# Kernel tuning notes

Hardware: AMD Instinct MI355X
Metric: run time of the kernel (lower is better)

The kernel has to match this reference:

```python
import jax, jax.numpy as jnp
import numpy as np
import math

SIZE = 64
NLAND = 8
N_ITER = 6


def setup_inputs() -> dict:
    key = jax.random.key(0)
    k1, k2, k3 = jax.random.split(key, 3)
    B, T, C = 4, 4096, 1024
    return {
        "q": jax.random.normal(k1, (B, T, C), dtype=jnp.float32),
        "k": jax.random.normal(k2, (B, T, C), dtype=jnp.float32),
        "v": jax.random.normal(k3, (B, T, C), dtype=jnp.float32),
    }


def _iterative_pinv(mat, n_iter=N_ITER):
    # Newton-Schulz iteration for pseudo-inverse of [..., m, m] kernel.
    m = mat.shape[-1]
    I = jnp.eye(m, dtype=mat.dtype)
    K = mat
    # NOTE: torch.max over the whole tensor (global scalar), faithful to source.
    V = (1.0 / jnp.max(jnp.sum(K, axis=-2))) * jnp.swapaxes(K, -1, -2)
    for _ in range(n_iter):
        KV = jnp.matmul(K, V)
        V = jnp.matmul(0.25 * V, 13.0 * I - jnp.matmul(KV, 15.0 * I - jnp.matmul(KV, 7.0 * I - KV)))
    return V


def reference(q, k, v):
    B, T, C = q.shape
    H = C // SIZE
    scale = 1.0 / math.sqrt(SIZE)
    # Faithful reshape (not transpose) as in the source module.
    qh = q.reshape(B, H, T, SIZE)
    kh = k.reshape(B, H, T, SIZE)
    vh = v.reshape(B, H, T, SIZE)
    # T % NLAND == 0 branch: landmark = segment mean over T//NLAND tokens.
    q_l = qh.reshape(B, H, NLAND, T // NLAND, SIZE).mean(axis=-2)  # [B,H,m,d]
    k_l = kh.reshape(B, H, NLAND, T // NLAND, SIZE).mean(axis=-2)
    kernel_1 = jax.nn.softmax(jnp.einsum('bhtd,bhmd->bhtm', qh, k_l) * scale, axis=-1)  # [B,H,T,m]
    kernel_2 = jax.nn.softmax(jnp.einsum('bhmd,bhnd->bhmn', q_l, k_l) * scale, axis=-1)  # [B,H,m,m]
    kernel_3 = jax.nn.softmax(jnp.einsum('bhmd,bhtd->bhmt', q_l, kh) * scale, axis=-1)  # [B,H,m,T]
    pinv = _iterative_pinv(kernel_2)  # [B,H,m,m]
    k3v = jnp.matmul(kernel_3, vh)    # [B,H,m,d]
    out = jnp.matmul(jnp.matmul(kernel_1, pinv), k3v)  # [B,H,T,d]
    return out.reshape(B, T, C)
```

## Files before the change

### kernel.cpp

```cpp
#include <hip/hip_runtime.h>
#include <math.h>

#define T_TOK 4096
#define DD 64
#define NHEADS 64
#define SEG 512
#define SCALE 0.125f

#define QL_OFF   0
#define KL_OFF   32768
#define K2_OFF   65536
#define CS_OFF   69632
#define KP_OFF   70144
#define PA_OFF   332288
#define PD_OFF   2429440
#define W2_OFF   2462208

#define WAVE_BAR() __builtin_amdgcn_wave_barrier()

__global__ __launch_bounds__(256) void qsum_kernel(
    const float* __restrict__ q, float* __restrict__ ws) {
  int tid = threadIdx.x;
  const float4* q4 = (const float4*)q + (size_t)blockIdx.x * 8192;
  float4 b[2][8];
#pragma unroll
  for (int i = 0; i < 8; ++i) b[0][i] = q4[i * 256 + tid];
  float4 a = make_float4(0.f, 0.f, 0.f, 0.f);
#pragma unroll
  for (int j = 0; j < 4; ++j) {
    if (j < 3) {
#pragma unroll
      for (int i = 0; i < 8; ++i)
        b[(j + 1) & 1][i] = q4[(j + 1) * 2048 + i * 256 + tid];
    }
#pragma unroll
    for (int i = 0; i < 8; ++i) {
      float4 x = b[j & 1][i];
      a.x += x.x; a.y += x.y; a.z += x.z; a.w += x.w;
    }
  }
  __shared__ float4 red[16][17];
  red[tid >> 4][tid & 15] = a;
  __syncthreads();
  if (tid < 16) {
    float4 s = make_float4(0.f, 0.f, 0.f, 0.f);
#pragma unroll
    for (int g = 0; g < 16; ++g) {
      float4 r = red[g][tid];
      s.x += r.x; s.y += r.y; s.z += r.z; s.w += r.w;
    }
    const float inv = 1.f / (float)SEG;
    s.x *= inv; s.y *= inv; s.z *= inv; s.w *= inv;
    ((float4*)(ws + QL_OFF))[blockIdx.x * 16 + tid] = s;
  }
}

__global__ __launch_bounds__(256) void kvpass_kernel(
    const float* __restrict__ k, const float* __restrict__ v,
    float* __restrict__ ws) {
  int tid = threadIdx.x;
  int w = tid >> 6, lane = tid & 63;
  int gw = blockIdx.x * 4 + w;
  int hb = gw >> 6;
  __shared__ float qls[8][68];
  __shared__ float kt_all[4][16][68];
  __shared__ float pl_all[4][16][9];
  float (*kt)[68] = kt_all[w];
  float (*pl)[9]  = pl_all[w];

  if (tid < 128) {
    float4 x = ((const float4*)(ws + QL_OFF))[hb * 128 + tid];
    *(float4*)&qls[tid >> 4][(tid & 15) * 4] = x;
  }
  __syncthreads();

  int m = lane & 7, g = lane >> 4;
  size_t tokbase = (size_t)gw * 64;
  const float4* k4 = (const float4*)k + tokbase * 16;
  const float4* v4 = (const float4*)v + tokbase * 16;
  float4 kb[2][4], vb[2][4];
#pragma unroll
  for (int i = 0; i < 4; ++i) { kb[0][i] = k4[i * 64 + lane]; vb[0][i] = v4[i * 64 + lane]; }

  float4 ks = make_float4(0.f, 0.f, 0.f, 0.f);
  float den = 0.f;
  float4 acc[8];
#pragma unroll
  for (int mm = 0; mm < 8; ++mm) acc[mm] = make_float4(0.f, 0.f, 0.f, 0.f);

#pragma unroll
  for (int tile = 0; tile < 4; ++tile) {
    int cur = tile & 1;
    if (tile < 3) {
#pragma unroll
      for (int i = 0; i < 4; ++i) {
        kb[cur ^ 1][i] = k4[(tile + 1) * 256 + i * 64 + lane];
        vb[cur ^ 1][i] = v4[(tile + 1) * 256 + i * 64 + lane];
      }
    }
#pragma unroll
    for (int i = 0; i < 4; ++i) {
      int f4 = i * 64 + lane;
      *(float4*)&kt[f4 >> 4][(f4 & 15) * 4] = kb[cur][i];
      ks.x += kb[cur][i].x; ks.y += kb[cur][i].y;
      ks.z += kb[cur][i].z; ks.w += kb[cur][i].w;
    }
    WAVE_BAR();
#pragma unroll
    for (int rep = 0; rep < 2; ++rep) {
      int t = rep * 8 + (lane >> 3);
      const float4* kr = (const float4*)&kt[t][0];
      const float4* qr = (const float4*)&qls[m][0];
      float dp = 0.f;
#pragma unroll
      for (int d4 = 0; d4 < 16; ++d4) {
        float4 kv = kr[d4], qv = qr[d4];
        dp += kv.x * qv.x + kv.y * qv.y + kv.z * qv.z + kv.w * qv.w;
      }
      float p = __expf(dp * SCALE);
      pl[t][m] = p;
      den += p;
    }
    WAVE_BAR();
#pragma unroll
    for (int i = 0; i < 4; ++i) {
      int t = i * 4 + g;
      float4 vv = vb[cur][i];
      float p0 = pl[t][0], p1 = pl[t][1], p2 = pl[t][2], p3 = pl[t][3];
      float p4 = pl[t][4], p5 = pl[t][5], p6 = pl[t][6], p7 = pl[t][7];
      acc[0].x += p0 * vv.x; acc[0].y += p0 * vv.y; acc[0].z += p0 * vv.z; acc[0].w += p0 * vv.w;
      acc[1].x += p1 * vv.x; acc[1].y += p1 * vv.y; acc[1].z += p1 * vv.z; acc[1].w += p1 * vv.w;
      acc[2].x += p2 * vv.x; acc[2].y += p2 * vv.y; acc[2].z += p2 * vv.z; acc[2].w += p2 * vv.w;
      acc[3].x += p3 * vv.x; acc[3].y += p3 * vv.y; acc[3].z += p3 * vv.z; acc[3].w += p3 * vv.w;
      acc[4].x += p4 * vv.x; acc[4].y += p4 * vv.y; acc[4].z += p4 * vv.z; acc[4].w += p4 * vv.w;
      acc[5].x += p5 * vv.x; acc[5].y += p5 * vv.y; acc[5].z += p5 * vv.z; acc[5].w += p5 * vv.w;
      acc[6].x += p6 * vv.x; acc[6].y += p6 * vv.y; acc[6].z += p6 * vv.z; acc[6].w += p6 * vv.w;
      acc[7].x += p7 * vv.x; acc[7].y += p7 * vv.y; acc[7].z += p7 * vv.z; acc[7].w += p7 * vv.w;
    }
    WAVE_BAR();
  }
  ks.x += __shfl_xor(ks.x, 16, 64); ks.y += __shfl_xor(ks.y, 16, 64);
  ks.z += __shfl_xor(ks.z, 16, 64); ks.w += __shfl_xor(ks.w, 16, 64);
  ks.x += __shfl_xor(ks.x, 32, 64); ks.y += __shfl_xor(ks.y, 32, 64);
  ks.z += __shfl_xor(ks.z, 32, 64); ks.w += __shfl_xor(ks.w, 32, 64);
  if (lane < 16)
    ((float4*)(ws + KP_OFF))[gw * 16 + lane] = ks;
  den += __shfl_xor(den, 8, 64);
  den += __shfl_xor(den, 16, 64);
  den += __shfl_xor(den, 32, 64);
  if (lane < 8)
    ws[PD_OFF + (size_t)gw * 8 + lane] = den;
#pragma unroll
  for (int mm = 0; mm < 8; ++mm) {
#pragma unroll
    for (int s = 16; s <= 32; s <<= 1) {
      acc[mm].x += __shfl_xor(acc[mm].x, s, 64);
      acc[mm].y += __shfl_xor(acc[mm].y, s, 64);
      acc[mm].z += __shfl_xor(acc[mm].z, s, 64);
      acc[mm].w += __shfl_xor(acc[mm].w, s, 64);
    }
  }
  if (lane < 16) {
#pragma unroll
    for (int mm = 0; mm < 8; ++mm)
      ((float4*)(ws + PA_OFF))[((size_t)gw * 8 + mm) * 16 + lane] = acc[mm];
  }
}

__global__ __launch_bounds__(512) void prepk_kernel(float* __restrict__ ws) {
  int hb = blockIdx.x, tid = threadIdx.x;
  __shared__ float qls[8][68];
  __shared__ float kls[8][68];
  __shared__ float ee[8][9];
  int m = tid >> 6, d = tid & 63;
  float s = 0.f;
#pragma unroll
  for (int j = 0; j < 8; ++j)
    s += ws[KP_OFF + (size_t)(hb * 64 + m * 8 + j) * 64 + d];
  s *= (1.f / (float)SEG);
  kls[m][d] = s;
  ws[KL_OFF + hb * 512 + tid] = s;
  qls[m][d] = ws[QL_OFF + hb * 512 + tid];
  __syncthreads();
  if (tid < 64) {
    int i = tid >> 3, j = tid & 7;
    float dot = 0.f;
#pragma unroll
    for (int dd = 0; dd < 64; ++dd) dot += qls[i][dd] * kls[j][dd];
    ee[i][j] = __expf(dot * SCALE);
  }
  __syncthreads();
  if (tid < 64) {
    int i = tid >> 3, j = tid & 7;
    float ssum = 0.f;
#pragma unroll
    for (int jj = 0; jj < 8; ++jj) ssum += ee[i][jj];
    ws[K2_OFF + hb * 64 + tid] = ee[i][j] / ssum;
  }
  if (tid < 8) {
    float cs = 0.f;
    for (int ii = 0; ii < 8; ++ii) {
      float ssum = 0.f;
#pragma unroll
      for (int jj = 0; jj < 8; ++jj) ssum += ee[ii][jj];
      cs += ee[ii][tid] / ssum;
    }
    ws[CS_OFF + hb * 8 + tid] = cs;
  }
}

__global__ __launch_bounds__(512) void pinvw2_kernel(float* __restrict__ ws) {
  int hb = blockIdx.x, tid = threadIdx.x;
  __shared__ float k3vs[8][68];
  __shared__ float K[8][9], V[8][9], X[8][9], Y[8][9];
  __shared__ float smax;
  int m = tid >> 6, d = tid & 63;
  float s = 0.f, den = 0.f;
  for (int c = 0; c < 64; ++c) {
    s += ws[PA_OFF + (((size_t)hb * 64 + c) * 8 + m) * 64 + d];
    den += ws[PD_OFF + ((size_t)hb * 64 + c) * 8 + m];
  }
  k3vs[m][d] = s / den;
  if (tid < 64) {
    float mx = 0.f;
    for (int t = 0; t < 8; ++t) mx = fmaxf(mx, ws[CS_OFF + t * 64 + tid]);
    for (int off = 32; off; off >>= 1) mx = fmaxf(mx, __shfl_xor(mx, off, 64));
    if (tid == 0) smax = mx;
  }
  int i = (tid >> 3) & 7, j = tid & 7;
  if (tid < 64) K[i][j] = ws[K2_OFF + hb * 64 + tid];
  __syncthreads();
  if (tid < 64) V[i][j] = K[j][i] * (1.f / smax);
  __syncthreads();
  for (int it = 0; it < 6; ++it) {
    float x = 0.f;
    if (tid < 64) {
      for (int kk = 0; kk < 8; ++kk) x += K[i][kk] * V[kk][j];
      X[i][j] = x;
    }
    __syncthreads();
    float bm = 0.f;
    if (tid < 64) {
      for (int kk = 0; kk < 8; ++kk) bm += X[i][kk] * X[kk][j];
      bm = 7.f * x - bm;
      Y[i][j] = bm;
    }
    __syncthreads();
    float dm = 0.f;
    if (tid < 64) {
      for (int kk = 0; kk < 8; ++kk) dm += X[i][kk] * Y[kk][j];
      dm = 15.f * x - dm;
    }
    __syncthreads();
    if (tid < 64) Y[i][j] = dm;
    __syncthreads();
    float vd = 0.f;
    if (tid < 64) {
      for (int kk = 0; kk < 8; ++kk) vd += V[i][kk] * Y[kk][j];
      vd = 0.25f * (13.f * V[i][j] - vd);
    }
    __syncthreads();
    if (tid < 64) V[i][j] = vd;
    __syncthreads();
  }
  float o = 0.f;
#pragma unroll
  for (int jj = 0; jj < 8; ++jj) o += V[m][jj] * k3vs[jj][d];
  ws[W2_OFF + hb * 512 + tid] = o;
}

__global__ __launch_bounds__(256) void out_kernel(
    const float* __restrict__ q, float* __restrict__ out,
    const float* __restrict__ ws) {
  int tid = threadIdx.x;
  int w = tid >> 6, lane = tid & 63;
  int gw = blockIdx.x * 4 + w;
  int hb = gw >> 6;
  __shared__ float qt_all[4][16][68];
  __shared__ float pl_all[4][16][9];
  __shared__ float w2_all[4][8][68];
  float (*qt)[68] = qt_all[w];
  float (*pl)[9]  = pl_all[w];
  float (*w2)[68] = w2_all[w];

  int m = lane & 7;
  float4 klrow[16];
#pragma unroll
  for (int d4 = 0; d4 < 16; ++d4)
    klrow[d4] = ((const float4*)(ws + KL_OFF))[hb * 128 + m * 16 + d4];
#pragma unroll
  for (int i = 0; i < 2; ++i) {
    int f4 = i * 64 + lane;
    float4 y = ((const float4*)(ws + W2_OFF))[hb * 128 + f4];
    *(float4*)&w2[f4 >> 4][(f4 & 15) * 4] = y;
  }

  size_t base4 = (size_t)gw * 1024;
  const float4* q4 = (const float4*)q + base4;
  float4* o4 = (float4*)out + base4;
  float4 buf[2][4];
#pragma unroll
  for (int i = 0; i < 4; ++i) buf[0][i] = q4[i * 64 + lane];

#pragma unroll
  for (int tile = 0; tile < 4; ++tile) {
    int cur = tile & 1;
    if (tile < 3) {
#pragma unroll
      for (int i = 0; i < 4; ++i)
        buf[cur ^ 1][i] = q4[(tile + 1) * 256 + i * 64 + lane];
    }
#pragma unroll
    for (int i = 0; i < 4; ++i) {
      int f4 = i * 64 + lane;
      *(float4*)&qt[f4 >> 4][(f4 & 15) * 4] = buf[cur][i];
    }
    WAVE_BAR();
#pragma unroll
    for (int rep = 0; rep < 2; ++rep) {
      int t = rep * 8 + (lane >> 3);
      const float4* qr = (const float4*)&qt[t][0];
      float dot = 0.f;
#pragma unroll
      for (int d4 = 0; d4 < 16; ++d4) {
        float4 a = qr[d4];
        dot += a.x * klrow[d4].x + a.y * klrow[d4].y +
               a.z * klrow[d4].z + a.w * klrow[d4].w;
      }
      pl[t][m] = __expf(dot * SCALE);
    }
    WAVE_BAR();
#pragma unroll
    for (int i = 0; i < 4; ++i) {
      int t = i * 4 + (lane >> 4);
      int qd = lane & 15;
      float p0 = pl[t][0], p1 = pl[t][1], p2 = pl[t][2], p3 = pl[t][3];
      float p4 = pl[t][4], p5 = pl[t][5], p6 = pl[t][6], p7 = pl[t][7];
      float inv = 1.f / (p0 + p1 + p2 + p3 + p4 + p5 + p6 + p7);
      float4 acc = make_float4(0.f, 0.f, 0.f, 0.f);
      float pm[8] = {p0, p1, p2, p3, p4, p5, p6, p7};
#pragma unroll
      for (int m2 = 0; m2 < 8; ++m2) {
        float wgt = pm[m2] * inv;
        float4 wv = *(const float4*)&w2[m2][qd * 4];
        acc.x += wgt * wv.x; acc.y += wgt * wv.y;
        acc.z += wgt * wv.z; acc.w += wgt * wv.w;
      }
      o4[tile * 256 + i * 64 + lane] = acc;
    }
    WAVE_BAR();
  }
}

extern "C" void kernel_launch(void* const* d_in, const int* in_sizes, int n_in,
                              void* d_out, int out_size, void* d_ws, size_t ws_size,
                              hipStream_t stream) {
  const float* q = (const float*)d_in[0];
  const float* k = (const float*)d_in[1];
  const float* v = (const float*)d_in[2];
  float* out = (float*)d_out;
  float* ws = (float*)d_ws;

  qsum_kernel<<<512, 256, 0, stream>>>(q, ws);
  kvpass_kernel<<<1024, 256, 0, stream>>>(k, v, ws);
  prepk_kernel<<<NHEADS, 512, 0, stream>>>(ws);
  pinvw2_kernel<<<NHEADS, 512, 0, stream>>>(ws);
  out_kernel<<<1024, 256, 0, stream>>>(q, out, ws);
}
```

Before: 99.14 us.

## Stage V through LDS and remap P·V accumulation to avoid cross-lane reductions

Result: slower. 116.6 us (+17.6%).

```diff
diff --git a/kernel.cpp b/kernel.cpp
--- a/kernel.cpp
+++ b/kernel.cpp
@@ -64,8 +64,10 @@
   int hb = gw >> 6;
   __shared__ float qls[8][68];
   __shared__ float kt_all[4][16][68];
+  __shared__ float vt_all[4][16][68];
   __shared__ float pl_all[4][16][9];
   float (*kt)[68] = kt_all[w];
+  float (*vt)[68] = vt_all[w];
   float (*pl)[9]  = pl_all[w];
 
   if (tid < 128) {
@@ -74,36 +76,35 @@
   }
   __syncthreads();
 
-  int m = lane & 7, g = lane >> 4;
+  int m = lane & 7, g = lane >> 4, d4i = lane & 15;
   size_t tokbase = (size_t)gw * 64;
   const float4* k4 = (const float4*)k + tokbase * 16;
   const float4* v4 = (const float4*)v + tokbase * 16;
-  float4 kb[2][4], vb[2][4];
-#pragma unroll
-  for (int i = 0; i < 4; ++i) { kb[0][i] = k4[i * 64 + lane]; vb[0][i] = v4[i * 64 + lane]; }
+
+  float4 kb[4], vb[4];
+#pragma unroll
+  for (int i = 0; i < 4; ++i) { kb[i] = k4[i * 64 + lane]; vb[i] = v4[i * 64 + lane]; }
 
   float4 ks = make_float4(0.f, 0.f, 0.f, 0.f);
   float den = 0.f;
-  float4 acc[8];
-#pragma unroll
-  for (int mm = 0; mm < 8; ++mm) acc[mm] = make_float4(0.f, 0.f, 0.f, 0.f);
+  float4 acc0 = make_float4(0.f, 0.f, 0.f, 0.f);
+  float4 acc1 = make_float4(0.f, 0.f, 0.f, 0.f);
 
 #pragma unroll
   for (int tile = 0; tile < 4; ++tile) {
-    int cur = tile & 1;
-    if (tile < 3) {
-#pragma unroll
-      for (int i = 0; i < 4; ++i) {
-        kb[cur ^ 1][i] = k4[(tile + 1) * 256 + i * 64 + lane];
-        vb[cur ^ 1][i] = v4[(tile + 1) * 256 + i * 64 + lane];
-      }
-    }
 #pragma unroll
     for (int i = 0; i < 4; ++i) {
       int f4 = i * 64 + lane;
-      *(float4*)&kt[f4 >> 4][(f4 & 15) * 4] = kb[cur][i];
-      ks.x += kb[cur][i].x; ks.y += kb[cur][i].y;
-      ks.z += kb[cur][i].z; ks.w += kb[cur][i].w;
+      *(float4*)&kt[f4 >> 4][(f4 & 15) * 4] = kb[i];
+      *(float4*)&vt[f4 >> 4][(f4 & 15) * 4] = vb[i];
+      ks.x += kb[i].x; ks.y += kb[i].y; ks.z += kb[i].z; ks.w += kb[i].w;
+    }
+    if (tile < 3) {
+#pragma unroll
+      for (int i = 0; i < 4; ++i) {
+        kb[i] = k4[(tile + 1) * 256 + i * 64 + lane];
+        vb[i] = v4[(tile + 1) * 256 + i * 64 + lane];
+      }
     }
     WAVE_BAR();
 #pragma unroll
@@ -123,19 +124,12 @@
     }
     WAVE_BAR();
 #pragma unroll
-    for (int i = 0; i < 4; ++i) {
-      int t = i * 4 + g;
-      float4 vv = vb[cur][i];
-      float p0 = pl[t][0], p1 = pl[t][1], p2 = pl[t][2], p3 = pl[t][3];
-      float p4 = pl[t][4], p5 = pl[t][5], p6 = pl[t][6], p7 = pl[t][7];
-      acc[0].x += p0 * vv.x; acc[0].y += p0 * vv.y; acc[0].z += p0 * vv.z; acc[0].w += p0 * vv.w;
-      acc[1].x += p1 * vv.x; acc[1].y += p1 * vv.y; acc[1].z += p1 * vv.z; acc[1].w += p1 * vv.w;
-      acc[2].x += p2 * vv.x; acc[2].y += p2 * vv.y; acc[2].z += p2 * vv.z; acc[2].w += p2 * vv.w;
-      acc[3].x += p3 * vv.x; acc[3].y += p3 * vv.y; acc[3].z += p3 * vv.z; acc[3].w += p3 * vv.w;
-      acc[4].x += p4 * vv.x; acc[4].y += p4 * vv.y; acc[4].z += p4 * vv.z; acc[4].w += p4 * vv.w;
-      acc[5].x += p5 * vv.x; acc[5].y += p5 * vv.y; acc[5].z += p5 * vv.z; acc[5].w += p5 * vv.w;
-      acc[6].x += p6 * vv.x; acc[6].y += p6 * vv.y; acc[6].z += p6 * vv.z; acc[6].w += p6 * vv.w;
-      acc[7].x += p7 * vv.x; acc[7].y += p7 * vv.y; acc[7].z += p7 * vv.z; acc[7].w += p7 * vv.w;
+    for (int t = 0; t < 16; ++t) {
+      float4 vv = *(const float4*)&vt[t][d4i * 4];
+      float pa = pl[t][g];
+      float pb = pl[t][g + 4];
+      acc0.x += pa * vv.x; acc0.y += pa * vv.y; acc0.z += pa * vv.z; acc0.w += pa * vv.w;
+      acc1.x += pb * vv.x; acc1.y += pb * vv.y; acc1.z += pb * vv.z; acc1.w += pb * vv.w;
     }
     WAVE_BAR();
   }
@@ -150,21 +144,8 @@
   den += __shfl_xor(den, 32, 64);
   if (lane < 8)
     ws[PD_OFF + (size_t)gw * 8 + lane] = den;
-#pragma unroll
-  for (int mm = 0; mm < 8; ++mm) {
-#pragma unroll
-    for (int s = 16; s <= 32; s <<= 1) {
-      acc[mm].x += __shfl_xor(acc[mm].x, s, 64);
-      acc[mm].y += __shfl_xor(acc[mm].y, s, 64);
-      acc[mm].z += __shfl_xor(acc[mm].z, s, 64);
-      acc[mm].w += __shfl_xor(acc[mm].w, s, 64);
-    }
-  }
-  if (lane < 16) {
-#pragma unroll
-    for (int mm = 0; mm < 8; ++mm)
-      ((float4*)(ws + PA_OFF))[((size_t)gw * 8 + mm) * 16 + lane] = acc[mm];
-  }
+  ((float4*)(ws + PA_OFF))[((size_t)gw * 8 + g) * 16 + d4i] = acc0;
+  ((float4*)(ws + PA_OFF))[((size_t)gw * 8 + g + 4) * 16 + d4i] = acc1;
 }
 
 __global__ __launch_bounds__(512) void prepk_kernel(float* __restrict__ ws) {
```
